# Performance work log

Hardware: AMD Instinct MI355X
Metric: run time of the kernel (lower is better)

The kernel has to match this reference:

```python
import jax, jax.numpy as jnp
import numpy as np

EPS_FEAT = 1.0 + 1e-4   # feature_map offset: elu(x) + 1.0 + 0.0001
EPS_DEN = 1e-6


def setup_inputs() -> dict:
    key = jax.random.key(0)
    k1, k2, k3 = jax.random.split(key, 3)
    B, L, D = 4, 4096, 1024
    x = jax.random.normal(k1, (B, L, D), dtype=jnp.float32)
    # torch Linear-style init scale ~ 1/sqrt(fan_in)
    W_qkv = jax.random.normal(k2, (D, 3 * D), dtype=jnp.float32) / np.sqrt(D)
    b_qkv = jnp.zeros((3 * D,), dtype=jnp.float32)
    W_out = jax.random.normal(k3, (D, D), dtype=jnp.float32) / np.sqrt(D)
    b_out = jnp.zeros((D,), dtype=jnp.float32)
    return {"x": x, "W_qkv": W_qkv, "b_qkv": b_qkv, "W_out": W_out, "b_out": b_out}


def _linear_attention(x, W_qkv, b_qkv, W_out, b_out, num_heads=16):
    B, L, D = x.shape
    H = num_heads
    E = D // H

    qkv = x @ W_qkv + b_qkv                       # (B, L, 3D)
    q, k, v = jnp.split(qkv, 3, axis=-1)
    q = q.reshape(B, L, H, E)
    k = k.reshape(B, L, H, E)
    v = v.reshape(B, L, H, E)

    q = jax.nn.elu(q * (E ** -0.5)) + EPS_FEAT    # scale BEFORE feature map (as in source)
    k = jax.nn.elu(k) + EPS_FEAT

    # Causal linear attention via recurrence over L; math identical to
    # cumsum of k \otimes v outer products, but never materializes (B,L,H,E,E).
    qL = jnp.moveaxis(q, 1, 0)                    # (L, B, H, E)
    kL = jnp.moveaxis(k, 1, 0)
    vL = jnp.moveaxis(v, 1, 0)

    kv0 = jnp.zeros((B, H, E, E), dtype=x.dtype)
    ks0 = jnp.zeros((B, H, E), dtype=x.dtype)

    def step(carry, qkv_t):
        kv_s, k_s = carry
        q_t, k_t, v_t = qkv_t                     # each (B, H, E)
        kv_s = kv_s + jnp.einsum('bhe,bhf->bhef', k_t, v_t)
        k_s = k_s + k_t
        num = jnp.einsum('bhe,bhef->bhf', q_t, kv_s)           # (B, H, E)
        den = jnp.einsum('bhe,bhe->bh', q_t, k_s)[..., None] + EPS_DEN
        return (kv_s, k_s), num / den

    _, out = jax.lax.scan(step, (kv0, ks0), (qL, kL, vL))       # out: (L, B, H, E)
    out = jnp.moveaxis(out, 0, 1).reshape(B, L, D)
    # dropout is identity in eval mode
    return out @ W_out + b_out


def reference(x, W_qkv, b_qkv, W_out, b_out):
    return _linear_attention(x, W_qkv, b_qkv, W_out, b_out)
```

## Files before the change

kernel.cpp:

```cpp
#include <hip/hip_runtime.h>
#include <hip/hip_bf16.h>
#include <stdint.h>

#define B_ 4
#define L_ 4096
#define D_ 1024
#define H_ 16
#define E_ 64
#define M_ (B_*L_)
#define N1_ (3*D_)
#define CHK 128
#define NC (L_/CHK)
#define BH (B_*H_)

#define EPS_FEAT 1.0001f
#define EPS_DEN 1e-6f

typedef __attribute__((ext_vector_type(4))) float f32x4;
typedef __attribute__((ext_vector_type(8))) short bf16x8;

__device__ __forceinline__ unsigned short f2bf(float x) {
    union { float f; unsigned int u; } v; v.f = x;
    unsigned int r = v.u + 0x7FFFu + ((v.u >> 16) & 1u);
    return (unsigned short)(r >> 16);
}

__device__ __forceinline__ void gload_lds16(const unsigned short* g, unsigned short* l) {
    __builtin_amdgcn_global_load_lds(
        (const __attribute__((address_space(1))) unsigned int*)(const void*)g,
        (__attribute__((address_space(3))) unsigned int*)(void*)l,
        16, 0, 0);
}


__global__ __launch_bounds__(256) void prep(const float* __restrict__ x,
                                            const float* __restrict__ W0,
                                            const float* __restrict__ W1,
                                            unsigned short* __restrict__ xb,
                                            unsigned short* __restrict__ T0,
                                            unsigned short* __restrict__ T1) {
    __shared__ float tile[32][33];
    int bid = blockIdx.x, t = threadIdx.x;
    if (bid < 16384) {
        int i4 = bid * 256 + t;
        float4 v = ((const float4*)x)[i4];
        unsigned int lo = (unsigned int)f2bf(v.x) | ((unsigned int)f2bf(v.y) << 16);
        unsigned int hi = (unsigned int)f2bf(v.z) | ((unsigned int)f2bf(v.w) << 16);
        ((uint2*)xb)[i4] = make_uint2(lo, hi);
        return;
    }
    const float* W; unsigned short* WT; int N, nb, kb;
    if (bid < 16384 + 3072) {
        int idx = bid - 16384;
        W = W0; WT = T0; N = N1_;
        nb = (idx % 96) * 32; kb = (idx / 96) * 32;
    } else {
        int idx = bid - 16384 - 3072;
        W = W1; WT = T1; N = D_;
        nb = (idx % 32) * 32; kb = (idx / 32) * 32;
    }
    int tx = t & 31, ty = t >> 5;
#pragma unroll
    for (int j = 0; j < 4; ++j)
        tile[ty + 8*j][tx] = W[(size_t)(kb + ty + 8*j) * N + nb + tx];
    __syncthreads();
#pragma unroll
    for (int j = 0; j < 4; ++j) {
        int nl = ty + 8*j;
        WT[(size_t)(nb + nl) * D_ + kb + tx] = f2bf(tile[tx][nl]);
    }
}


template<int MODE, int KDIM, int NDIM>
__global__ __launch_bounds__(256, 2) void gemm128(
    const unsigned short* __restrict__ A,
    const unsigned short* __restrict__ BT,
    const float* __restrict__ bias,
    float* __restrict__ outF,
    unsigned short* __restrict__ qf,
    unsigned short* __restrict__ kf,
    unsigned short* __restrict__ vf)
{
    __shared__ __align__(16) unsigned short smem[36864];

    const int t = threadIdx.x, lane = t & 63, w = t >> 6;

    const int nwgx = NDIM / 256;
    const int nwg = nwgx * (M_ / 128);
    const int bid0 = blockIdx.y * nwgx + blockIdx.x;
    const int swz = (bid0 & 7) * (nwg >> 3) + (bid0 >> 3);
    const int m0 = (swz / nwgx) * 128, n0 = (swz % nwgx) * 256;
    const int lr = lane & 15, lg = lane >> 4;

    auto stage = [&](int T) {
        unsigned short* base = smem + (T % 3) * 12288;
        const int kt = T * 32;
#pragma unroll
        for (int i = 0; i < 2; ++i) {
            int c = i * 256 + t;
            int row = c >> 2, s = c & 3;
            int col = ((s ^ ((row >> 1) & 3)) << 3);
            gload_lds16(A + (size_t)(m0 + row) * KDIM + kt + col, &base[c * 8]);
        }
        unsigned short* bb = base + 4096;
#pragma unroll
        for (int i = 0; i < 4; ++i) {
            int c = i * 256 + t;
            int row = c >> 2, s = c & 3;
            int col = ((s ^ ((row >> 1) & 3)) << 3);
            gload_lds16(BT + (size_t)(n0 + row) * KDIM + kt + col, &bb[c * 8]);
        }
    };

    f32x4 acc[8][4] = {};

    auto tile = [&](int T, bool s1) {
        const unsigned short* Ab = smem + (T % 3) * 12288;
        const unsigned short* Bb = Ab + 4096;
        bf16x8 af[8], bq[4];
#pragma unroll
        for (int m = 0; m < 8; ++m) {
            int row = m * 16 + lr;
            int slot = lg ^ ((row >> 1) & 3);
            af[m] = *(const bf16x8*)&Ab[row * 32 + slot * 8];
        }
#pragma unroll
        for (int n = 0; n < 4; ++n) {
            int row = w * 64 + n * 16 + lr;
            int slot = lg ^ ((row >> 1) & 3);
            bq[n] = *(const bf16x8*)&Bb[row * 32 + slot * 8];
        }
        if (s1) stage(T + 2);
        __builtin_amdgcn_s_barrier();
        asm volatile("s_waitcnt lgkmcnt(0)" ::: "memory");
        __builtin_amdgcn_sched_barrier(0);
        __builtin_amdgcn_s_setprio(1);
#pragma unroll
        for (int m = 0; m < 8; ++m)
#pragma unroll
            for (int n = 0; n < 4; ++n)
                acc[m][n] = __builtin_amdgcn_mfma_f32_16x16x32_bf16(af[m], bq[n], acc[m][n], 0, 0, 0);
        __builtin_amdgcn_s_setprio(0);
    };

    constexpr int NT = KDIM / 32;
    stage(0); stage(1);
    asm volatile("s_waitcnt vmcnt(6)" ::: "memory");
    __builtin_amdgcn_s_barrier();
    __builtin_amdgcn_sched_barrier(0);

    for (int T = 0; T < NT - 2; ++T) {
        tile(T, true);
        asm volatile("s_waitcnt vmcnt(6)" ::: "memory");
        __builtin_amdgcn_s_barrier();
        __builtin_amdgcn_sched_barrier(0);
    }
    tile(NT - 2, false);
    asm volatile("s_waitcnt vmcnt(0)" ::: "memory");
    __builtin_amdgcn_s_barrier();
    __builtin_amdgcn_sched_barrier(0);
    tile(NT - 1, false);
    __syncthreads();

    if (MODE == 0) {
        unsigned short* cbf = smem;
        const bool isQ = (n0 < D_), isK = (n0 >= D_ && n0 < 2*D_);
        const float scale = isQ ? 0.125f : 1.0f;
        unsigned short* buf = isQ ? qf : (isK ? kf : vf);
        const int b = m0 >> 12, l0 = m0 & 4095;
        const int h0 = (n0 & 1023) >> 6;
#pragma unroll
        for (int n = 0; n < 4; ++n) {
            int cl = w*64 + n*16 + lr;
            float bv = bias[n0 + cl];
#pragma unroll
            for (int m = 0; m < 8; ++m)
#pragma unroll
                for (int q = 0; q < 4; ++q) {
                    int rl = m*16 + lg*4 + q;
                    float val = (acc[m][n][q] + bv) * scale;
                    float fv = (isQ || isK)
                               ? ((val > 0.f ? val : __expf(val) - 1.f) + EPS_FEAT)
                               : val;
                    cbf[rl * 264 + cl] = f2bf(fv);
                }
        }
        __syncthreads();
#pragma unroll
        for (int hh = 0; hh < 4; ++hh) {
            unsigned short* dst = buf + (((size_t)(b * H_ + h0 + hh)) * L_ + l0) * E_;
#pragma unroll
            for (int i = 0; i < 4; ++i) {
                int c = i*256 + t, row = c >> 3, ch = c & 7;
                uint4 v = *(const uint4*)&cbf[row * 264 + hh*64 + ch*8];
                *(uint4*)&dst[row * 64 + ch*8] = v;
            }
        }
    } else {
        float* cfl = (float*)smem;
#pragma unroll
        for (int p = 0; p < 2; ++p) {
#pragma unroll
            for (int n = 0; n < 4; ++n) {
                int cl = w*64 + n*16 + lr;
                float bv = bias[n0 + cl];
#pragma unroll
                for (int mm = 0; mm < 4; ++mm)
#pragma unroll
                    for (int q = 0; q < 4; ++q) {
                        int rl = mm*16 + lg*4 + q;
                        cfl[rl * 260 + cl] = acc[p*4 + mm][n][q] + bv;
                    }
            }
            __syncthreads();
#pragma unroll
            for (int i = 0; i < 16; ++i) {
                int c = i*256 + t, row = c >> 6, ch = c & 63;
                float4 v = *(const float4*)&cfl[row * 260 + ch*4];
                *(float4*)&outF[(size_t)(m0 + p*64 + row) * NDIM + n0 + ch*4] = v;
            }
            __syncthreads();
        }
    }
}


__global__ __launch_bounds__(256) void chunk_kv(
    const unsigned short* __restrict__ kf, const unsigned short* __restrict__ vf,
    unsigned short* __restrict__ kvout, float* __restrict__ ksout)
{
    constexpr int LDK = 136;
    __shared__ unsigned short Kt[64 * LDK];
    __shared__ unsigned short Vt[80 * LDK];

    int t = threadIdx.x, lane = t & 63, w = t >> 6;
    int bid = blockIdx.x;
    const unsigned short* kp = kf + (size_t)bid * CHK * E_;
    const unsigned short* vp = vf + (size_t)bid * CHK * E_;

#pragma unroll
    for (int it = 0; it < 4; ++it) {
        int s = it * 256 + t;
        int rl = s >> 3, e0 = (s & 7) << 3;
        uint4 kv8 = *(const uint4*)(kp + s * 8);
        uint4 vv8 = *(const uint4*)(vp + s * 8);
        unsigned int kw[4] = {kv8.x, kv8.y, kv8.z, kv8.w};
        unsigned int vw[4] = {vv8.x, vv8.y, vv8.z, vv8.w};
#pragma unroll
        for (int jw = 0; jw < 4; ++jw) {
            Kt[(e0 + 2*jw    ) * LDK + rl] = (unsigned short)(kw[jw] & 0xFFFF);
            Kt[(e0 + 2*jw + 1) * LDK + rl] = (unsigned short)(kw[jw] >> 16);
            Vt[(e0 + 2*jw    ) * LDK + rl] = (unsigned short)(vw[jw] & 0xFFFF);
            Vt[(e0 + 2*jw + 1) * LDK + rl] = (unsigned short)(vw[jw] >> 16);
        }
    }
    if (t < 128) Vt[64 * LDK + t] = 0x3F80;
    for (int i = t; i < 15 * LDK; i += 256) Vt[65 * LDK + i] = 0;
    __syncthreads();

    int lr = lane & 15, lg = lane >> 4;
    f32x4 acc[4] = {};
    f32x4 accE[4] = {};
#pragma unroll
    for (int ks = 0; ks < 4; ++ks) {
        bf16x8 a = *(const bf16x8*)&Vt[(w*16 + lr) * LDK + ks*32 + lg*8];
#pragma unroll
        for (int n = 0; n < 4; ++n) {
            bf16x8 b = *(const bf16x8*)&Kt[(n*16 + lr) * LDK + ks*32 + lg*8];
            acc[n] = __builtin_amdgcn_mfma_f32_16x16x32_bf16(a, b, acc[n], 0, 0, 0);
        }
    }
    if (w == 0) {
#pragma unroll
        for (int ks = 0; ks < 4; ++ks) {
            bf16x8 a = *(const bf16x8*)&Vt[(64 + lr) * LDK + ks*32 + lg*8];
#pragma unroll
            for (int n = 0; n < 4; ++n) {
                bf16x8 b = *(const bf16x8*)&Kt[(n*16 + lr) * LDK + ks*32 + lg*8];
                accE[n] = __builtin_amdgcn_mfma_f32_16x16x32_bf16(a, b, accE[n], 0, 0, 0);
            }
        }
    }
    unsigned short* kvo = kvout + (size_t)bid * E_ * E_;
#pragma unroll
    for (int n = 0; n < 4; ++n)
#pragma unroll
        for (int q = 0; q < 4; ++q) {
            int f = w*16 + lg*4 + q, e = n*16 + lr;
            kvo[f * 64 + e] = f2bf(acc[n][q]);
        }
    if (w == 0 && lg == 0) {
#pragma unroll
        for (int n = 0; n < 4; ++n)
            ksout[(size_t)bid * 64 + n*16 + lr] = accE[n][0];
    }
}


__global__ __launch_bounds__(256) void prefix_kv(
    const uint2* __restrict__ kvin, const float* __restrict__ ks,
    uint2* __restrict__ kvb, unsigned short* __restrict__ ksb)
{
    int bh = blockIdx.y, part = blockIdx.x, t = threadIdx.x;
    int idx = part * 256 + t;
    float st0 = 0.f, st1 = 0.f, st2 = 0.f, st3 = 0.f;
    for (int c = 0; c < NC; ++c) {
        size_t o = ((size_t)bh * NC + c) * 1024 + idx;
        uint2 tmp = kvin[o];
        kvb[o] = make_uint2(
            (unsigned int)f2bf(st0) | ((unsigned int)f2bf(st1) << 16),
            (unsigned int)f2bf(st2) | ((unsigned int)f2bf(st3) << 16));
        union { unsigned int u; float f; } cv;
        cv.u = (tmp.x & 0xFFFFu) << 16; st0 += cv.f;
        cv.u = tmp.x & 0xFFFF0000u;     st1 += cv.f;
        cv.u = (tmp.y & 0xFFFFu) << 16; st2 += cv.f;
        cv.u = tmp.y & 0xFFFF0000u;     st3 += cv.f;
    }
    if (part == 0 && t < 64) {
        float s0 = 0.f;
        for (int c = 0; c < NC; ++c) {
            float tmp = ks[((size_t)bh * NC + c) * 64 + t];
            ksb[((size_t)bh * NC + c) * 64 + t] = f2bf(s0);
            s0 += tmp;
        }
    }
}


__global__ __launch_bounds__(256, 2) void attn_out(
    const unsigned short* __restrict__ qf, const unsigned short* __restrict__ kf,
    const unsigned short* __restrict__ vf, const unsigned short* __restrict__ kvb,
    const unsigned short* __restrict__ ksb, unsigned short* __restrict__ attn)
{
    constexpr int LK = 72;
    constexpr int LV = 136;
    __shared__ unsigned short Ks[128 * LK];
    __shared__ unsigned short Vt[64 * LV];
    __shared__ unsigned short Ss[128 * LV];

    int t = threadIdx.x, lane = t & 63, w = t >> 6;
    int bid = blockIdx.x;
    int bh = bid >> 5, c = bid & 31;
    const unsigned short* qp = qf + (size_t)bid * CHK * E_;
    const unsigned short* kp = kf + (size_t)bid * CHK * E_;
    const unsigned short* vp = vf + (size_t)bid * CHK * E_;
    const unsigned short* kvp = kvb + (size_t)bid * 4096;

    int lr = lane & 15, lg = lane >> 4;
    const int jsel[2] = {w, 7 - w};

    bf16x8 aq[2][2];
#pragma unroll
    for (int mi = 0; mi < 2; ++mi)
#pragma unroll
        for (int ks = 0; ks < 2; ++ks)
            aq[mi][ks] = *(const bf16x8*)(qp + (jsel[mi]*16 + lr) * 64 + ks*32 + lg*8);

#pragma unroll
    for (int it = 0; it < 4; ++it) {
        int s = it * 256 + t;
        int r = s >> 3, e0 = (s & 7) << 3;
        uint4 kv = *(const uint4*)(kp + s * 8);
        uint4 vv = *(const uint4*)(vp + s * 8);
        *(uint4*)&Ks[r * LK + e0] = kv;
        unsigned int vw[4] = {vv.x, vv.y, vv.z, vv.w};
#pragma unroll
        for (int jw = 0; jw < 4; ++jw) {
            Vt[(e0 + 2*jw    ) * LV + r] = (unsigned short)(vw[jw] & 0xFFFF);
            Vt[(e0 + 2*jw + 1) * LV + r] = (unsigned short)(vw[jw] >> 16);
        }
    }
    bf16x8 zfrag = {0,0,0,0,0,0,0,0};
    bf16x8 bone = zfrag, bks[2] = {zfrag, zfrag};
    if (lr == 0) {
#pragma unroll
        for (int j = 0; j < 8; ++j) bone[j] = (short)0x3F80;
        bks[0] = *(const bf16x8*)&ksb[(size_t)bid * 64 + lg*8];
        bks[1] = *(const bf16x8*)&ksb[(size_t)bid * 64 + 32 + lg*8];
    }
    __syncthreads();

#pragma unroll
    for (int mi = 0; mi < 2; ++mi) {
        int j = jsel[mi];
        int rbase = j * 16;
        int jbmax = j | 1;
        for (int jb = 0; jb <= jbmax; ++jb) {
            if (jb <= j) {
                f32x4 sacc = {};
                bf16x8 b0 = *(const bf16x8*)&Ks[(jb*16 + lr) * LK + lg*8];
                bf16x8 b1 = *(const bf16x8*)&Ks[(jb*16 + lr) * LK + 32 + lg*8];
                sacc = __builtin_amdgcn_mfma_f32_16x16x32_bf16(aq[mi][0], b0, sacc, 0, 0, 0);
                sacc = __builtin_amdgcn_mfma_f32_16x16x32_bf16(aq[mi][1], b1, sacc, 0, 0, 0);
#pragma unroll
                for (int q = 0; q < 4; ++q) {
                    int r = rbase + lg*4 + q;
                    int jj = jb*16 + lr;
                    Ss[r * LV + jj] = (jj <= r) ? f2bf(sacc[q]) : (unsigned short)0;
                }
            } else {
#pragma unroll
                for (int q = 0; q < 4; ++q) {
                    int r = rbase + lg*4 + q;
                    Ss[r * LV + jb*16 + lr] = 0;
                }
            }
        }
    }

    f32x4 oacc[2][5] = {};
#pragma unroll
    for (int mi = 0; mi < 2; ++mi) {
        int j = jsel[mi];
        int rbase = j * 16;
#pragma unroll
        for (int ks = 0; ks < 2; ++ks) {
            bf16x8 a = aq[mi][ks];
#pragma unroll
            for (int n = 0; n < 4; ++n) {
                bf16x8 b = *(const bf16x8*)&kvp[(n*16 + lr) * 64 + ks*32 + lg*8];
                oacc[mi][n] = __builtin_amdgcn_mfma_f32_16x16x32_bf16(a, b, oacc[mi][n], 0, 0, 0);
            }
            oacc[mi][4] = __builtin_amdgcn_mfma_f32_16x16x32_bf16(a, bks[ks], oacc[mi][4], 0, 0, 0);
        }
        for (int ks = 0; ks <= (j >> 1); ++ks) {
            bf16x8 a = *(const bf16x8*)&Ss[(rbase + lr) * LV + ks*32 + lg*8];
#pragma unroll
            for (int n = 0; n < 4; ++n) {
                bf16x8 b = *(const bf16x8*)&Vt[(n*16 + lr) * LV + ks*32 + lg*8];
                oacc[mi][n] = __builtin_amdgcn_mfma_f32_16x16x32_bf16(a, b, oacc[mi][n], 0, 0, 0);
            }
            oacc[mi][4] = __builtin_amdgcn_mfma_f32_16x16x32_bf16(a, bone, oacc[mi][4], 0, 0, 0);
        }
    }

    int b_idx = bh >> 4, h_idx = bh & 15;
#pragma unroll
    for (int mi = 0; mi < 2; ++mi) {
        int rbase = jsel[mi] * 16;
        float den[4];
#pragma unroll
        for (int q = 0; q < 4; ++q)
            den[q] = __shfl(oacc[mi][4][q], lane & 48, 64) + EPS_DEN;
#pragma unroll
        for (int n = 0; n < 4; ++n) {
#pragma unroll
            for (int q = 0; q < 4; ++q) {
                int r = rbase + lg*4 + q;
                int lpos = c * CHK + r;
                int col = n*16 + lr;
                size_t dst = ((size_t)b_idx * L_ + lpos) * D_ + h_idx * 64 + col;
                attn[dst] = f2bf(oacc[mi][n][q] / den[q]);
            }
        }
    }
}


extern "C" void kernel_launch(void* const* d_in, const int* in_sizes, int n_in,
                              void* d_out, int out_size, void* d_ws, size_t ws_size,
                              hipStream_t stream)
{
    const float* x    = (const float*)d_in[0];
    const float* Wqkv = (const float*)d_in[1];
    const float* bqkv = (const float*)d_in[2];
    const float* Wout = (const float*)d_in[3];
    const float* bout = (const float*)d_in[4];
    float* out = (float*)d_out;

    char* ws = (char*)d_ws;
    size_t off = 0;
    auto alloc = [&](size_t bytes) { void* p = ws + off; off += (bytes + 255) & ~(size_t)255; return p; };
    unsigned short* xb  = (unsigned short*)alloc((size_t)M_ * D_ * 2);
    unsigned short* WqT = (unsigned short*)alloc((size_t)N1_ * D_ * 2);
    unsigned short* WoT = (unsigned short*)alloc((size_t)D_ * D_ * 2);
    unsigned short* qfb = (unsigned short*)alloc((size_t)M_ * D_ * 2);
    unsigned short* kfb = (unsigned short*)alloc((size_t)M_ * D_ * 2);
    unsigned short* vfb = (unsigned short*)alloc((size_t)M_ * D_ * 2);
    unsigned short* kvw = (unsigned short*)alloc((size_t)BH * NC * E_ * E_ * 2);
    float* ksw = (float*)alloc((size_t)BH * NC * E_ * 4);
    unsigned short* kvb = (unsigned short*)alloc((size_t)BH * NC * E_ * E_ * 2);
    unsigned short* ksb = (unsigned short*)alloc((size_t)BH * NC * E_ * 2);
    unsigned short* attn = xb;

    prep<<<16384 + 3072 + 1024, 256, 0, stream>>>(x, Wqkv, Wout, xb, WqT, WoT);

    gemm128<0, D_, N1_><<<dim3(N1_ / 256, M_ / 128), 256, 0, stream>>>(
        xb, WqT, bqkv, nullptr, qfb, kfb, vfb);

    chunk_kv<<<BH * NC, 256, 0, stream>>>(kfb, vfb, kvw, ksw);
    prefix_kv<<<dim3(4, BH), 256, 0, stream>>>((const uint2*)kvw, ksw, (uint2*)kvb, ksb);
    attn_out<<<BH * NC, 256, 0, stream>>>(qfb, kfb, vfb, kvb, ksb, attn);

    gemm128<1, D_, D_><<<dim3(D_ / 256, M_ / 128), 256, 0, stream>>>(
        attn, WoT, bout, out, nullptr, nullptr, nullptr);
}
```

Before: 235.3 us.

## Fuse fp32-to-bf16 conversion of x into QKV GEMM A-tile loading

Removes the separate x-to-bf16 conversion pass from the prep kernel. The QKV GEMM instead loads fp32 A rows into registers, converts them, and writes bf16 into swizzled LDS, software-pipelined one stage ahead. This saves one write and one read of the bf16 copy of x, at the cost of reading fp32 A in every GEMM column block (12 N-blocks), which doubles the A bytes fetched per tile and adds conversion ALU work plus register pressure in the mainloop. It also adds a dead mfma_phase lambda.

```diff
diff --git a/kernel.cpp b/kernel.cpp
--- a/kernel.cpp
+++ b/kernel.cpp
@@ -33,29 +33,18 @@
 }
 
 
-__global__ __launch_bounds__(256) void prep(const float* __restrict__ x,
-                                            const float* __restrict__ W0,
+__global__ __launch_bounds__(256) void prep(const float* __restrict__ W0,
                                             const float* __restrict__ W1,
-                                            unsigned short* __restrict__ xb,
                                             unsigned short* __restrict__ T0,
                                             unsigned short* __restrict__ T1) {
     __shared__ float tile[32][33];
     int bid = blockIdx.x, t = threadIdx.x;
-    if (bid < 16384) {
-        int i4 = bid * 256 + t;
-        float4 v = ((const float4*)x)[i4];
-        unsigned int lo = (unsigned int)f2bf(v.x) | ((unsigned int)f2bf(v.y) << 16);
-        unsigned int hi = (unsigned int)f2bf(v.z) | ((unsigned int)f2bf(v.w) << 16);
-        ((uint2*)xb)[i4] = make_uint2(lo, hi);
-        return;
-    }
     const float* W; unsigned short* WT; int N, nb, kb;
-    if (bid < 16384 + 3072) {
-        int idx = bid - 16384;
+    if (bid < 3072) {
         W = W0; WT = T0; N = N1_;
-        nb = (idx % 96) * 32; kb = (idx / 96) * 32;
+        nb = (bid % 96) * 32; kb = (bid / 96) * 32;
     } else {
-        int idx = bid - 16384 - 3072;
+        int idx = bid - 3072;
         W = W1; WT = T1; N = D_;
         nb = (idx % 32) * 32; kb = (idx / 32) * 32;
     }
@@ -74,7 +63,7 @@
 
 template<int MODE, int KDIM, int NDIM>
 __global__ __launch_bounds__(256, 2) void gemm128(
-    const unsigned short* __restrict__ A,
+    const void* __restrict__ Araw,
     const unsigned short* __restrict__ BT,
     const float* __restrict__ bias,
     float* __restrict__ outF,
@@ -93,17 +82,12 @@
     const int m0 = (swz / nwgx) * 128, n0 = (swz % nwgx) * 256;
     const int lr = lane & 15, lg = lane >> 4;
 
-    auto stage = [&](int T) {
-        unsigned short* base = smem + (T % 3) * 12288;
+    const float* Af = (const float*)Araw;
+    const unsigned short* Ab16 = (const unsigned short*)Araw;
+
+    auto stageB = [&](int T) {
+        unsigned short* bb = smem + (T % 3) * 12288 + 4096;
         const int kt = T * 32;
-#pragma unroll
-        for (int i = 0; i < 2; ++i) {
-            int c = i * 256 + t;
-            int row = c >> 2, s = c & 3;
-            int col = ((s ^ ((row >> 1) & 3)) << 3);
-            gload_lds16(A + (size_t)(m0 + row) * KDIM + kt + col, &base[c * 8]);
-        }
-        unsigned short* bb = base + 4096;
 #pragma unroll
         for (int i = 0; i < 4; ++i) {
             int c = i * 256 + t;
@@ -112,10 +96,50 @@
             gload_lds16(BT + (size_t)(n0 + row) * KDIM + kt + col, &bb[c * 8]);
         }
     };
+    auto stageA1 = [&](int T) {
+        unsigned short* base = smem + (T % 3) * 12288;
+        const int kt = T * 32;
+#pragma unroll
+        for (int i = 0; i < 2; ++i) {
+            int c = i * 256 + t;
+            int row = c >> 2, s = c & 3;
+            int col = ((s ^ ((row >> 1) & 3)) << 3);
+            gload_lds16(Ab16 + (size_t)(m0 + row) * KDIM + kt + col, &base[c * 8]);
+        }
+    };
+
+    uint4 areg[4];
+    auto loadA0 = [&](int T) {
+        const int kt = T * 32;
+#pragma unroll
+        for (int i = 0; i < 2; ++i) {
+            int c = i * 256 + t;
+            int row = c >> 2, s = c & 3;
+            const float* src = Af + (size_t)(m0 + row) * KDIM + kt + s * 8;
+            areg[i*2]   = *(const uint4*)src;
+            areg[i*2+1] = *(const uint4*)(src + 4);
+        }
+    };
+    auto writeA0 = [&](int T) {
+        unsigned short* base = smem + (T % 3) * 12288;
+#pragma unroll
+        for (int i = 0; i < 2; ++i) {
+            int c = i * 256 + t;
+            int row = c >> 2, s = c & 3;
+            int slot = s ^ ((row >> 1) & 3);
+            const float* f = (const float*)&areg[i * 2];
+            uint4 wv;
+            wv.x = (unsigned int)f2bf(f[0]) | ((unsigned int)f2bf(f[1]) << 16);
+            wv.y = (unsigned int)f2bf(f[2]) | ((unsigned int)f2bf(f[3]) << 16);
+            wv.z = (unsigned int)f2bf(f[4]) | ((unsigned int)f2bf(f[5]) << 16);
+            wv.w = (unsigned int)f2bf(f[6]) | ((unsigned int)f2bf(f[7]) << 16);
+            *(uint4*)&base[row * 32 + slot * 8] = wv;
+        }
+    };
 
     f32x4 acc[8][4] = {};
 
-    auto tile = [&](int T, bool s1) {
+    auto mfma_phase = [&](int T) {
         const unsigned short* Ab = smem + (T % 3) * 12288;
         const unsigned short* Bb = Ab + 4096;
         bf16x8 af[8], bq[4];
@@ -131,7 +155,35 @@
             int slot = lg ^ ((row >> 1) & 3);
             bq[n] = *(const bf16x8*)&Bb[row * 32 + slot * 8];
         }
-        if (s1) stage(T + 2);
+        return [=, &acc]() mutable {};
+    };
+    (void)mfma_phase;
+
+    constexpr int NT = KDIM / 32;
+
+    auto tile = [&](int T, bool wA, bool lA, bool sB) {
+        const unsigned short* Ab = smem + (T % 3) * 12288;
+        const unsigned short* Bb = Ab + 4096;
+        bf16x8 af[8], bq[4];
+#pragma unroll
+        for (int m = 0; m < 8; ++m) {
+            int row = m * 16 + lr;
+            int slot = lg ^ ((row >> 1) & 3);
+            af[m] = *(const bf16x8*)&Ab[row * 32 + slot * 8];
+        }
+#pragma unroll
+        for (int n = 0; n < 4; ++n) {
+            int row = w * 64 + n * 16 + lr;
+            int slot = lg ^ ((row >> 1) & 3);
+            bq[n] = *(const bf16x8*)&Bb[row * 32 + slot * 8];
+        }
+        if (MODE == 0) {
+            if (wA) writeA0(T + 2);
+            if (lA) loadA0(T + 3);
+            if (sB) stageB(T + 2);
+        } else {
+            if (sB) { stageA1(T + 2); stageB(T + 2); }
+        }
         __builtin_amdgcn_s_barrier();
         asm volatile("s_waitcnt lgkmcnt(0)" ::: "memory");
         __builtin_amdgcn_sched_barrier(0);
@@ -144,23 +196,47 @@
         __builtin_amdgcn_s_setprio(0);
     };
 
-    constexpr int NT = KDIM / 32;
-    stage(0); stage(1);
-    asm volatile("s_waitcnt vmcnt(6)" ::: "memory");
-    __builtin_amdgcn_s_barrier();
-    __builtin_amdgcn_sched_barrier(0);
-
-    for (int T = 0; T < NT - 2; ++T) {
-        tile(T, true);
+    if (MODE == 0) {
+        loadA0(0); writeA0(0);
+        loadA0(1); writeA0(1);
+        loadA0(2);
+        stageB(0); stageB(1);
+        asm volatile("s_waitcnt vmcnt(0)" ::: "memory");
+        __builtin_amdgcn_s_barrier();
+        __builtin_amdgcn_sched_barrier(0);
+        for (int T = 0; T <= NT - 4; ++T) {
+            tile(T, true, true, true);
+            asm volatile("s_waitcnt vmcnt(8)" ::: "memory");
+            __builtin_amdgcn_s_barrier();
+            __builtin_amdgcn_sched_barrier(0);
+        }
+        tile(NT - 3, true, false, true);
+        asm volatile("s_waitcnt vmcnt(4)" ::: "memory");
+        __builtin_amdgcn_s_barrier();
+        __builtin_amdgcn_sched_barrier(0);
+        tile(NT - 2, false, false, false);
+        asm volatile("s_waitcnt vmcnt(0)" ::: "memory");
+        __builtin_amdgcn_s_barrier();
+        __builtin_amdgcn_sched_barrier(0);
+        tile(NT - 1, false, false, false);
+    } else {
+        stageA1(0); stageB(0);
+        stageA1(1); stageB(1);
         asm volatile("s_waitcnt vmcnt(6)" ::: "memory");
         __builtin_amdgcn_s_barrier();
         __builtin_amdgcn_sched_barrier(0);
-    }
-    tile(NT - 2, false);
-    asm volatile("s_waitcnt vmcnt(0)" ::: "memory");
-    __builtin_amdgcn_s_barrier();
-    __builtin_amdgcn_sched_barrier(0);
-    tile(NT - 1, false);
+        for (int T = 0; T < NT - 2; ++T) {
+            tile(T, false, false, true);
+            asm volatile("s_waitcnt vmcnt(6)" ::: "memory");
+            __builtin_amdgcn_s_barrier();
+            __builtin_amdgcn_sched_barrier(0);
+        }
+        tile(NT - 2, false, false, false);
+        asm volatile("s_waitcnt vmcnt(0)" ::: "memory");
+        __builtin_amdgcn_s_barrier();
+        __builtin_amdgcn_sched_barrier(0);
+        tile(NT - 1, false, false, false);
+    }
     __syncthreads();
 
     if (MODE == 0) {
@@ -472,7 +548,6 @@
     char* ws = (char*)d_ws;
     size_t off = 0;
     auto alloc = [&](size_t bytes) { void* p = ws + off; off += (bytes + 255) & ~(size_t)255; return p; };
-    unsigned short* xb  = (unsigned short*)alloc((size_t)M_ * D_ * 2);
     unsigned short* WqT = (unsigned short*)alloc((size_t)N1_ * D_ * 2);
     unsigned short* WoT = (unsigned short*)alloc((size_t)D_ * D_ * 2);
     unsigned short* qfb = (unsigned short*)alloc((size_t)M_ * D_ * 2);
@@ -482,12 +557,12 @@
     float* ksw = (float*)alloc((size_t)BH * NC * E_ * 4);
     unsigned short* kvb = (unsigned short*)alloc((size_t)BH * NC * E_ * E_ * 2);
     unsigned short* ksb = (unsigned short*)alloc((size_t)BH * NC * E_ * 2);
-    unsigned short* attn = xb;
-
-    prep<<<16384 + 3072 + 1024, 256, 0, stream>>>(x, Wqkv, Wout, xb, WqT, WoT);
+    unsigned short* attn = (unsigned short*)alloc((size_t)M_ * D_ * 2);
+
+    prep<<<3072 + 1024, 256, 0, stream>>>(Wqkv, Wout, WqT, WoT);
 
     gemm128<0, D_, N1_><<<dim3(N1_ / 256, M_ / 128), 256, 0, stream>>>(
-        xb, WqT, bqkv, nullptr, qfb, kfb, vfb);
+        x, WqT, bqkv, nullptr, qfb, kfb, vfb);
 
     chunk_kv<<<BH * NC, 256, 0, stream>>>(kfb, vfb, kvw, ksw);
     prefix_kv<<<dim3(4, BH), 256, 0, stream>>>((const uint2*)kvw, ksw, (uint2*)kvb, ksb);
```

After: 249.6 us. +6.1%, slower.
